# Kernel tuning notes

Measured on AMD Instinct MI355X. Metric: run time of the kernel, lower is better.

The kernel has to match this reference:

```python
import jax, jax.numpy as jnp
import numpy as np

B, L, D, H = 4, 2048, 2048, 16
HEAD_DIM = D // H
EPS = 1e-5


def rmsnorm(x, w):
    # fp32 RMSNorm as in the torch module
    xf = x.astype(jnp.float32)
    rms = jnp.sqrt(jnp.mean(xf * xf, axis=-1, keepdims=True) + EPS)
    return xf / rms * w


def apply_rope(x, freqs):
    # x: (..., D) with interleaved even/odd pairs; freqs: (2, L, D/2) = (sin, cos)
    sin, cos = freqs[0], freqs[1]
    xr = x.reshape(*x.shape[:-1], D // 2, 2)
    x_even, x_odd = xr[..., 0], xr[..., 1]
    e = x_even * cos - x_odd * sin
    o = x_odd * cos + x_even * sin
    return jnp.stack([e, o], axis=-1).reshape(x.shape)


def setup_inputs() -> dict:
    key = jax.random.key(0)
    k0, k1, k2 = jax.random.split(key, 3)
    x_BLD = jax.random.normal(k0, (B, L, D), dtype=jnp.float32)
    # realistic RoPE angle table over the full dim (matches module usage)
    t = jnp.arange(L, dtype=jnp.float32)[:, None]
    inv_freq = 1.0 / (10000.0 ** (jnp.arange(D // 2, dtype=jnp.float32) / (D // 2)))
    ang = t * inv_freq[None, :]                      # (L, D/2)
    freqs = jnp.stack([jnp.sin(ang), jnp.cos(ang)])  # (2, L, D/2)
    wqkv = jax.random.normal(k1, (3 * D, D), dtype=jnp.float32) * 0.02
    wo = jax.random.normal(k2, (D, D), dtype=jnp.float32) * 0.02
    q_norm_w = jnp.ones((D,), dtype=jnp.float32)
    k_norm_w = jnp.ones((D,), dtype=jnp.float32)
    return {"x_BLD": x_BLD, "freqs": freqs, "wqkv": wqkv, "wo": wo,
            "q_norm_w": q_norm_w, "k_norm_w": k_norm_w}


def reference(x_BLD, freqs, wqkv, wo, q_norm_w, k_norm_w):
    dtype = x_BLD.dtype
    qkv = x_BLD @ wqkv.T                             # (B, L, 3D)
    q, k, v = jnp.split(qkv, 3, axis=-1)
    q = apply_rope(rmsnorm(q, q_norm_w), freqs).astype(dtype)
    k = apply_rope(rmsnorm(k, k_norm_w), freqs).astype(dtype)
    # (B, L, D) -> (B, H, L, hd)
    q = q.reshape(B, L, H, HEAD_DIM).transpose(0, 2, 1, 3)
    k = k.reshape(B, L, H, HEAD_DIM).transpose(0, 2, 1, 3)
    v = v.reshape(B, L, H, HEAD_DIM).transpose(0, 2, 1, 3)
    scale = HEAD_DIM ** -0.5
    scores = jnp.einsum('bhqd,bhkd->bhqk', q, k) * scale
    attn = jax.nn.softmax(scores, axis=-1)
    out = jnp.einsum('bhqk,bhkd->bhqd', attn, v)
    out = out.transpose(0, 2, 1, 3).reshape(B, L, D)
    return out @ wo.T
```

## Files before the change

kernel.cpp:

```cpp
#include <hip/hip_runtime.h>
#include <stdint.h>
#include <stddef.h>

typedef unsigned short u16;
typedef __bf16 bf16x8 __attribute__((ext_vector_type(8)));
typedef float  f32x4  __attribute__((ext_vector_type(4)));
typedef float  f32x16 __attribute__((ext_vector_type(16)));

__device__ __forceinline__ float bf2f(u16 u){ return __uint_as_float(((unsigned)u)<<16); }
__device__ __forceinline__ u16 f2bf(float f){
  unsigned u = __float_as_uint(f);
  return (u16)((u + 0x7fffu + ((u>>16)&1u)) >> 16);
}
__device__ __forceinline__ void gl_lds16(const void* g, void* s){
  __builtin_amdgcn_global_load_lds(
      (__attribute__((address_space(1))) void*)(void*)g,
      (__attribute__((address_space(3))) void*)s, 16, 0, 0);
}

__global__ void k_f2bf(const float* __restrict__ in, u16* __restrict__ out, int n4){
  int i = blockIdx.x*256 + threadIdx.x;
  if (i < n4){
    float4 v = ((const float4*)in)[i];
    ((ushort4*)out)[i] = make_ushort4(f2bf(v.x), f2bf(v.y), f2bf(v.z), f2bf(v.w));
  }
}

template<int BF16OUT>
__global__ __launch_bounds__(256,2) void k_gemm_bt(const u16* __restrict__ A,
                                                   const u16* __restrict__ Bm,
                                                   void* __restrict__ Cout,
                                                   int M, int N, int K){
  __shared__ __align__(16) u16 As[128*64];
  __shared__ __align__(16) u16 Bs[128*64];
  const int tid = threadIdx.x, w = tid>>6, ln = tid&63;
  const int l16 = ln&15, quad = ln>>4;
  const int wm = w&1, wn = w>>1;
  const int m0 = blockIdx.y*128, n0 = blockIdx.x*128;
  const f32x4 z4 = {0.f,0.f,0.f,0.f};
  f32x4 acc[4][4];
  #pragma unroll
  for (int i=0;i<4;++i)
    #pragma unroll
    for (int j=0;j<4;++j) acc[i][j] = z4;

  const int nkb = K >> 6;
  for (int kb=0; kb<nkb; ++kb){
    __syncthreads();
    const int ka = kb*64;
    #pragma unroll
    for (int j=0;j<4;++j){
      gl_lds16(A  + (size_t)(m0 + w*32 + j*8 + (ln>>3))*K + ka + (ln&7)*8,
               &As[(w*32+j*8)*64]);
      gl_lds16(Bm + (size_t)(n0 + w*32 + j*8 + (ln>>3))*K + ka + (ln&7)*8,
               &Bs[(w*32+j*8)*64]);
    }
    __builtin_amdgcn_s_waitcnt(0);
    __syncthreads();
    #pragma unroll
    for (int k0=0;k0<64;k0+=32){
      bf16x8 a[4], b[4];
      #pragma unroll
      for (int mt=0;mt<4;++mt) a[mt] = *(const bf16x8*)&As[(wm*64+mt*16+l16)*64 + k0 + quad*8];
      #pragma unroll
      for (int nt=0;nt<4;++nt) b[nt] = *(const bf16x8*)&Bs[(wn*64+nt*16+l16)*64 + k0 + quad*8];
      #pragma unroll
      for (int mt=0;mt<4;++mt)
        #pragma unroll
        for (int nt=0;nt<4;++nt)
          acc[mt][nt] = __builtin_amdgcn_mfma_f32_16x16x32_bf16(a[mt], b[nt], acc[mt][nt], 0,0,0);
    }
  }
  #pragma unroll
  for (int mt=0;mt<4;++mt)
    #pragma unroll
    for (int nt=0;nt<4;++nt)
      #pragma unroll
      for (int j=0;j<4;++j){
        int row = m0 + wm*64 + mt*16 + quad*4 + j;
        int col = n0 + wn*64 + nt*16 + l16;
        if (BF16OUT) ((u16*)Cout)[(size_t)row*N + col] = f2bf(acc[mt][nt][j]);
        else         ((float*)Cout)[(size_t)row*N + col] = acc[mt][nt][j];
      }
}

__global__ void k_prep_qk(const u16* __restrict__ qkv, const float* __restrict__ freqs,
                          const float* __restrict__ qw, const float* __restrict__ kw,
                          u16* __restrict__ Qo, u16* __restrict__ Ko){
  const int row = blockIdx.x;
  const int b = row >> 11, l = row & 2047;
  const int tid = threadIdx.x;
  const u16* qr = qkv + (size_t)row*6144;
  float qe[4], qo[4], ke[4], ko_[4];
  float sq = 0.f, sk = 0.f;
  #pragma unroll
  for (int it=0; it<4; ++it){
    int p = tid + it*256;
    ushort2 q2 = ((const ushort2*)qr)[p];
    ushort2 k2 = ((const ushort2*)(qr+2048))[p];
    qe[it]=bf2f(q2.x); qo[it]=bf2f(q2.y);
    ke[it]=bf2f(k2.x); ko_[it]=bf2f(k2.y);
    sq += qe[it]*qe[it] + qo[it]*qo[it];
    sk += ke[it]*ke[it] + ko_[it]*ko_[it];
  }
  #pragma unroll
  for (int off=32; off; off>>=1){ sq += __shfl_xor(sq, off); sk += __shfl_xor(sk, off); }
  __shared__ float red[8];
  if ((tid&63)==0){ red[tid>>6]=sq; red[4+(tid>>6)]=sk; }
  __syncthreads();
  sq = red[0]+red[1]+red[2]+red[3];
  sk = red[4]+red[5]+red[6]+red[7];
  const float rq = rsqrtf(sq*(1.f/2048.f) + 1e-5f);
  const float rk = rsqrtf(sk*(1.f/2048.f) + 1e-5f);
  const float QS = 0.08838834764831845f * 1.4426950408889634f;
  #pragma unroll
  for (int it=0; it<4; ++it){
    int p = tid + it*256;
    float sn = freqs[(size_t)l*1024 + p];
    float cs = freqs[2097152 + (size_t)l*1024 + p];
    float2 w2q = ((const float2*)qw)[p];
    float2 w2k = ((const float2*)kw)[p];
    int h = p>>6, dd2 = p&63;
    size_t o = ((size_t)(b*16+h)*2048 + l)*64 + dd2;
    float a = qe[it]*rq*w2q.x, c = qo[it]*rq*w2q.y;
    ((ushort2*)Qo)[o] = make_ushort2(f2bf((a*cs - c*sn)*QS), f2bf((c*cs + a*sn)*QS));
    a = ke[it]*rk*w2k.x; c = ko_[it]*rk*w2k.y;
    ((ushort2*)Ko)[o] = make_ushort2(f2bf(a*cs - c*sn), f2bf(c*cs + a*sn));
  }
}

__global__ void k_prep_v(const u16* __restrict__ qkv, u16* __restrict__ Vt){
  const int lt = blockIdx.x, bh = blockIdx.y;
  const int b = bh>>4, h = bh&15;
  __shared__ u16 tile[64][136];
  const int tid = threadIdx.x;
  #pragma unroll
  for (int it=0; it<32; ++it){
    int idx = it*256 + tid;
    int lo = idx >> 7, dd = idx & 127;
    tile[lo][dd] = qkv[(size_t)(b*2048 + lt*64 + lo)*6144 + 4096 + h*128 + dd];
  }
  __syncthreads();
  #pragma unroll
  for (int it=0; it<32; ++it){
    int idx = it*256 + tid;
    int dd = idx >> 6, lo = idx & 63;
    Vt[((size_t)bh*128 + dd)*2048 + lt*64 + lo] = tile[lo][dd];
  }
}

__global__ __launch_bounds__(256,2) void k_flash(const u16* __restrict__ Q,
                                                 const u16* __restrict__ Kg,
                                                 const u16* __restrict__ Vt,
                                                 u16* __restrict__ O){
  __shared__ __align__(16) u16 Kt[128*136];
  __shared__ __align__(16) u16 Vs[128*136];
  const int qt = blockIdx.x, bh = blockIdx.y;
  const int tid = threadIdx.x, w = tid>>6, ln = tid&63;
  const int l31 = ln&31, hi = ln>>5;
  const int b = bh>>4, h = bh&15;
  const size_t qkbase = (size_t)bh*(2048*128);

  const int srow = tid>>4, scol = tid&15;
  const u16* kgp = Kg + qkbase + (size_t)srow*128 + scol*8;
  const u16* vgp = Vt + (size_t)bh*(128*2048) + (size_t)srow*2048 + scol*8;
  u16* kld = &Kt[srow*136 + scol*8];
  u16* vld = &Vs[srow*136 + scol*8];

  bf16x8 qf[8];
  {
    const u16* qp = Q + qkbase + (size_t)(qt*128 + w*32 + l31)*128 + hi*8;
    #pragma unroll
    for (int kk=0; kk<8; ++kk) qf[kk] = *(const bf16x8*)(qp + kk*16);
  }

  f32x16 o[4];
  #pragma unroll
  for (int dt=0; dt<4; ++dt)
    #pragma unroll
    for (int r=0; r<16; ++r) o[dt][r] = 0.f;
  float l_ = 0.f;

  bf16x8 kreg[8], vreg[8];
  #pragma unroll
  for (int it=0; it<8; ++it) kreg[it] = *(const bf16x8*)(kgp + (size_t)it*16*128);
  #pragma unroll
  for (int it=0; it<8; ++it) vreg[it] = *(const bf16x8*)(vgp + (size_t)it*16*2048);

  union U4 { unsigned u[4]; bf16x8 v; };

  for (int kt=0; kt<16; ++kt){
    __syncthreads();
    #pragma unroll
    for (int it=0; it<8; ++it) *(bf16x8*)(kld + it*16*136) = kreg[it];
    #pragma unroll
    for (int it=0; it<8; ++it) *(bf16x8*)(vld + it*16*136) = vreg[it];
    __syncthreads();
    if (kt < 15){
      #pragma unroll
      for (int it=0; it<8; ++it)
        kreg[it] = *(const bf16x8*)(kgp + (size_t)(kt+1)*128*128 + (size_t)it*16*128);
      #pragma unroll
      for (int it=0; it<8; ++it)
        vreg[it] = *(const bf16x8*)(vgp + (kt+1)*128 + (size_t)it*16*2048);
    }
    f32x16 s[4];
    #pragma unroll
    for (int t=0;t<4;++t)
      #pragma unroll
      for (int r=0;r<16;++r) s[t][r] = 0.f;
    #pragma unroll
    for (int kk=0; kk<8; ++kk){
      #pragma unroll
      for (int t=0; t<4; ++t){
        bf16x8 a = *(const bf16x8*)&Kt[(t*32 + l31)*136 + kk*16 + hi*8];
        s[t] = __builtin_amdgcn_mfma_f32_32x32x16_bf16(a, qf[kk], s[t], 0,0,0);
      }
    }
    float rs = 0.f;
    bf16x8 bfrag[8];
    #pragma unroll
    for (int t=0;t<4;++t){
      unsigned pk[4][2];
      #pragma unroll
      for (int g=0;g<4;++g){
        float p0 = exp2f(s[t][g*4+0] - 8.0f);
        float p1 = exp2f(s[t][g*4+1] - 8.0f);
        float p2 = exp2f(s[t][g*4+2] - 8.0f);
        float p3 = exp2f(s[t][g*4+3] - 8.0f);
        rs += (p0+p1)+(p2+p3);
        pk[g][0] = (unsigned)f2bf(p0) | ((unsigned)f2bf(p1)<<16);
        pk[g][1] = (unsigned)f2bf(p2) | ((unsigned)f2bf(p3)<<16);
      }
      unsigned a0 = (unsigned)__shfl_xor((int)(hi ? pk[0][0] : pk[1][0]), 32);
      unsigned a1 = (unsigned)__shfl_xor((int)(hi ? pk[0][1] : pk[1][1]), 32);
      unsigned b0 = (unsigned)__shfl_xor((int)(hi ? pk[2][0] : pk[3][0]), 32);
      unsigned b1 = (unsigned)__shfl_xor((int)(hi ? pk[2][1] : pk[3][1]), 32);
      U4 u0, u1;
      u0.u[0] = hi ? a0       : pk[0][0];
      u0.u[1] = hi ? a1       : pk[0][1];
      u0.u[2] = hi ? pk[1][0] : a0;
      u0.u[3] = hi ? pk[1][1] : a1;
      u1.u[0] = hi ? b0       : pk[2][0];
      u1.u[1] = hi ? b1       : pk[2][1];
      u1.u[2] = hi ? pk[3][0] : b0;
      u1.u[3] = hi ? pk[3][1] : b1;
      bfrag[t*2+0] = u0.v;
      bfrag[t*2+1] = u1.v;
    }
    rs += __shfl_xor(rs, 32);
    l_ += rs;
    #pragma unroll
    for (int kk=0; kk<8; ++kk){
      #pragma unroll
      for (int dt=0; dt<4; ++dt){
        bf16x8 a = *(const bf16x8*)&Vs[(dt*32 + l31)*136 + kk*16 + hi*8];
        o[dt] = __builtin_amdgcn_mfma_f32_32x32x16_bf16(a, bfrag[kk], o[dt], 0,0,0);
      }
    }
  }
  const float inv = 1.f/l_;
  __syncthreads();
  #pragma unroll
  for (int dt=0;dt<4;++dt)
    #pragma unroll
    for (int g=0;g<4;++g)
      *(ushort4*)&Kt[(w*32+l31)*136 + dt*32 + g*8 + hi*4] =
        make_ushort4(f2bf(o[dt][g*4+0]*inv), f2bf(o[dt][g*4+1]*inv),
                     f2bf(o[dt][g*4+2]*inv), f2bf(o[dt][g*4+3]*inv));
  __syncthreads();
  #pragma unroll
  for (int it=0; it<8; ++it){
    int q = it*16 + srow;
    bf16x8 vv = *(const bf16x8*)&Kt[q*136 + scol*8];
    *(bf16x8*)&O[(size_t)(b*2048 + qt*128 + q)*2048 + h*128 + scol*8] = vv;
  }
}

extern "C" void kernel_launch(void* const* d_in, const int* in_sizes, int n_in,
                              void* d_out, int out_size, void* d_ws, size_t ws_size,
                              hipStream_t stream){
  const float* x     = (const float*)d_in[0];
  const float* freqs = (const float*)d_in[1];
  const float* wqkv  = (const float*)d_in[2];
  const float* wo    = (const float*)d_in[3];
  const float* qw    = (const float*)d_in[4];
  const float* kw    = (const float*)d_in[5];
  char* ws = (char*)d_ws;
  u16* xbf    = (u16*)(ws);
  u16* wqkvbf = (u16*)(ws + 33554432);
  u16* wobf   = (u16*)(ws + 58720256);
  u16* qkvbf  = (u16*)(ws + 67108864);
  u16* Qbf    = (u16*)(ws + 167772160);
  u16* Kbf    = (u16*)(ws + 201326592);
  u16* Vtbf   = (u16*)(ws + 234881024);
  u16* Abf    = qkvbf;
  float* out  = (float*)d_out;

  k_f2bf<<<16384,256,0,stream>>>(x,    xbf,    4194304);
  k_f2bf<<<12288,256,0,stream>>>(wqkv, wqkvbf, 3145728);
  k_f2bf<<< 4096,256,0,stream>>>(wo,   wobf,   1048576);
  k_gemm_bt<1><<<dim3(48,64),256,0,stream>>>(xbf, wqkvbf, qkvbf, 8192, 6144, 2048);
  k_prep_qk<<<8192,256,0,stream>>>(qkvbf, freqs, qw, kw, Qbf, Kbf);
  k_prep_v<<<dim3(32,64),256,0,stream>>>(qkvbf, Vtbf);
  k_flash<<<dim3(16,64),256,0,stream>>>(Qbf, Kbf, Vtbf, Abf);
  k_gemm_bt<0><<<dim3(16,64),256,0,stream>>>(Abf, wobf, out, 8192, 2048, 2048);
}
```

Measured before the change: 740.9 us.

## Replace GEMM with 256x256-tile, 8-wave, double-buffered pipelined kernel

Replaces the 128x128 single-buffered bf16 GEMM with a 256x256 tile kernel using 512 threads. Global-to-LDS loads of the next K slices are interleaved with MFMA work on quarter-tiles, using partial vmcnt waits and barriers. The LDS layout is XOR-swizzled to avoid bank conflicts, workgroup order is remapped for L2 locality, and MFMA issue priority is raised with s_setprio. The cost targeted is the load/compute serialisation and low reuse of the old loop. In exchange it uses 128KB of LDS per block and a more fragile barrier schedule.

Result: faster. 698.2 us (-5.8%).

```diff
diff --git a/kernel.cpp b/kernel.cpp
--- a/kernel.cpp
+++ b/kernel.cpp
@@ -26,62 +26,115 @@
   }
 }
 
+#define BAR()  do{ __asm__ __volatile__("" ::: "memory"); \
+                   __builtin_amdgcn_s_barrier(); \
+                   __asm__ __volatile__("" ::: "memory"); }while(0)
+#define LGKM0() __asm__ __volatile__("s_waitcnt lgkmcnt(0)" ::: "memory")
+#define VMC4()  __asm__ __volatile__("s_waitcnt vmcnt(4)" ::: "memory")
+#define VMC0()  __asm__ __volatile__("s_waitcnt vmcnt(0)" ::: "memory")
+
+#define STAGE_A(B_,H_,T_) do{ \
+  const u16* _s = A + (size_t)(m0 + (H_)*128 + w16 + sr)*K + (T_)*64 + sc; \
+  gl_lds16(_s,               &As[B_][H_][w16*64]); \
+  gl_lds16(_s + (size_t)8*K, &As[B_][H_][(w16+8)*64]); }while(0)
+#define STAGE_B(B_,H_,T_) do{ \
+  const u16* _s = Bm + (size_t)(n0 + (H_)*128 + w16 + sr)*K + (T_)*64 + sc; \
+  gl_lds16(_s,               &Bs[B_][H_][w16*64]); \
+  gl_lds16(_s + (size_t)8*K, &Bs[B_][H_][(w16+8)*64]); }while(0)
+
+#define RD_A(H_,B_) do{ \
+  _Pragma("unroll") for (int mt=0; mt<4; ++mt){ \
+    int r_ = wm*64 + mt*16 + l16; const u16* p_ = &As[B_][H_][r_*64]; \
+    af[mt][0] = *(const bf16x8*)&p_[(( quad    ^ (r_&7))<<3)]; \
+    af[mt][1] = *(const bf16x8*)&p_[(((quad+4) ^ (r_&7))<<3)]; } }while(0)
+#define RD_B(H_,B_) do{ \
+  _Pragma("unroll") for (int nt=0; nt<2; ++nt){ \
+    int r_ = wn*32 + nt*16 + l16; const u16* p_ = &Bs[B_][H_][r_*64]; \
+    bfr[nt][0] = *(const bf16x8*)&p_[(( quad    ^ (r_&7))<<3)]; \
+    bfr[nt][1] = *(const bf16x8*)&p_[(((quad+4) ^ (r_&7))<<3)]; } }while(0)
+
+#define MM(QM,QN) do{ \
+  LGKM0(); \
+  __builtin_amdgcn_s_setprio(1); \
+  _Pragma("unroll") for (int k_=0;k_<2;++k_) \
+    _Pragma("unroll") for (int mt=0;mt<4;++mt) \
+      _Pragma("unroll") for (int nt=0;nt<2;++nt) \
+        acc[QM][QN][mt][nt] = __builtin_amdgcn_mfma_f32_16x16x32_bf16( \
+            af[mt][k_], bfr[nt][k_], acc[QM][QN][mt][nt], 0,0,0); \
+  __builtin_amdgcn_s_setprio(0); }while(0)
+
 template<int BF16OUT>
-__global__ __launch_bounds__(256,2) void k_gemm_bt(const u16* __restrict__ A,
+__global__ __launch_bounds__(512,2) void k_gemm256(const u16* __restrict__ A,
                                                    const u16* __restrict__ Bm,
                                                    void* __restrict__ Cout,
                                                    int M, int N, int K){
-  __shared__ __align__(16) u16 As[128*64];
-  __shared__ __align__(16) u16 Bs[128*64];
+  __shared__ __align__(16) u16 As[2][2][128*64];
+  __shared__ __align__(16) u16 Bs[2][2][128*64];
   const int tid = threadIdx.x, w = tid>>6, ln = tid&63;
   const int l16 = ln&15, quad = ln>>4;
   const int wm = w&1, wn = w>>1;
-  const int m0 = blockIdx.y*128, n0 = blockIdx.x*128;
-  const f32x4 z4 = {0.f,0.f,0.f,0.f};
-  f32x4 acc[4][4];
-  #pragma unroll
-  for (int i=0;i<4;++i)
-    #pragma unroll
-    for (int j=0;j<4;++j) acc[i][j] = z4;
-
-  const int nkb = K >> 6;
-  for (int kb=0; kb<nkb; ++kb){
-    __syncthreads();
-    const int ka = kb*64;
-    #pragma unroll
-    for (int j=0;j<4;++j){
-      gl_lds16(A  + (size_t)(m0 + w*32 + j*8 + (ln>>3))*K + ka + (ln&7)*8,
-               &As[(w*32+j*8)*64]);
-      gl_lds16(Bm + (size_t)(n0 + w*32 + j*8 + (ln>>3))*K + ka + (ln&7)*8,
-               &Bs[(w*32+j*8)*64]);
-    }
-    __builtin_amdgcn_s_waitcnt(0);
-    __syncthreads();
-    #pragma unroll
-    for (int k0=0;k0<64;k0+=32){
-      bf16x8 a[4], b[4];
-      #pragma unroll
-      for (int mt=0;mt<4;++mt) a[mt] = *(const bf16x8*)&As[(wm*64+mt*16+l16)*64 + k0 + quad*8];
-      #pragma unroll
-      for (int nt=0;nt<4;++nt) b[nt] = *(const bf16x8*)&Bs[(wn*64+nt*16+l16)*64 + k0 + quad*8];
+  const int w16 = w*16, sr = ln>>3;
+  const int sc = ((ln&7) ^ sr) << 3;
+  const int nbx = N>>8;
+  const int nwg = nbx*(M>>8);
+  const int lid = blockIdx.y*nbx + blockIdx.x;
+  const int swz = (lid&7)*(nwg>>3) + (lid>>3);
+  const int m0 = (swz/nbx)<<8, n0 = (swz%nbx)<<8;
+
+  f32x4 acc[2][2][4][2];
+  #pragma unroll
+  for (int a=0;a<2;++a)
+    #pragma unroll
+    for (int b=0;b<2;++b)
+      #pragma unroll
+      for (int c=0;c<4;++c)
+        #pragma unroll
+        for (int d=0;d<2;++d){ acc[a][b][c][d][0]=0.f; acc[a][b][c][d][1]=0.f;
+                               acc[a][b][c][d][2]=0.f; acc[a][b][c][d][3]=0.f; }
+  bf16x8 af[4][2], bfr[2][2];
+
+  STAGE_A(0,0,0); STAGE_B(0,0,0); STAGE_A(0,1,0); STAGE_B(0,1,0);
+  STAGE_B(1,0,1); STAGE_A(1,1,1);
+  VMC4(); BAR();
+
+  const int niter = K>>7;
+  for (int j=0; j<niter-1; ++j){
+    const int t1 = 2*j+1;
+    RD_A(0,0); RD_B(0,0); STAGE_A(1,0,t1);           BAR(); MM(0,0); BAR();
+    RD_A(1,0);            STAGE_B(1,1,t1);           BAR(); MM(1,0); BAR();
+    RD_B(1,0);            STAGE_B(0,0,t1+1);         BAR(); MM(1,1); BAR();
+    RD_A(0,0);            STAGE_A(0,1,t1+1); VMC4(); BAR(); MM(0,1); BAR();
+    RD_A(0,1); RD_B(0,1); STAGE_A(0,0,t1+1);         BAR(); MM(0,0); BAR();
+    RD_A(1,1);            STAGE_B(0,1,t1+1);         BAR(); MM(1,0); BAR();
+    RD_B(1,1);            STAGE_B(1,0,t1+2);         BAR(); MM(1,1); BAR();
+    RD_A(0,1);            STAGE_A(1,1,t1+2); VMC4(); BAR(); MM(0,1); BAR();
+  }
+  {
+    const int T1 = 2*niter-1;
+    RD_A(0,0); RD_B(0,0); STAGE_A(1,0,T1);           BAR(); MM(0,0); BAR();
+    RD_A(1,0);            STAGE_B(1,1,T1);           BAR(); MM(1,0); BAR();
+    RD_B(1,0);                                       BAR(); MM(1,1); BAR();
+    RD_A(0,0);                               VMC0(); BAR(); MM(0,1); BAR();
+    RD_A(0,1); RD_B(0,1);                            BAR(); MM(0,0); BAR();
+    RD_A(1,1);                                       BAR(); MM(1,0); BAR();
+    RD_B(1,1);                                       BAR(); MM(1,1); BAR();
+    RD_A(0,1);                                       BAR(); MM(0,1); BAR();
+  }
+  #pragma unroll
+  for (int qm=0;qm<2;++qm)
+    #pragma unroll
+    for (int qn=0;qn<2;++qn)
       #pragma unroll
       for (int mt=0;mt<4;++mt)
         #pragma unroll
-        for (int nt=0;nt<4;++nt)
-          acc[mt][nt] = __builtin_amdgcn_mfma_f32_16x16x32_bf16(a[mt], b[nt], acc[mt][nt], 0,0,0);
-    }
-  }
-  #pragma unroll
-  for (int mt=0;mt<4;++mt)
-    #pragma unroll
-    for (int nt=0;nt<4;++nt)
-      #pragma unroll
-      for (int j=0;j<4;++j){
-        int row = m0 + wm*64 + mt*16 + quad*4 + j;
-        int col = n0 + wn*64 + nt*16 + l16;
-        if (BF16OUT) ((u16*)Cout)[(size_t)row*N + col] = f2bf(acc[mt][nt][j]);
-        else         ((float*)Cout)[(size_t)row*N + col] = acc[mt][nt][j];
-      }
+        for (int nt=0;nt<2;++nt)
+          #pragma unroll
+          for (int jj=0;jj<4;++jj){
+            int row = m0 + qm*128 + wm*64 + mt*16 + quad*4 + jj;
+            int col = n0 + qn*128 + wn*32 + nt*16 + l16;
+            if (BF16OUT) ((u16*)Cout)[(size_t)row*N + col] = f2bf(acc[qm][qn][mt][nt][jj]);
+            else         ((float*)Cout)[(size_t)row*N + col] = acc[qm][qn][mt][nt][jj];
+          }
 }
 
 __global__ void k_prep_qk(const u16* __restrict__ qkv, const float* __restrict__ freqs,
@@ -300,9 +353,9 @@
   k_f2bf<<<16384,256,0,stream>>>(x,    xbf,    4194304);
   k_f2bf<<<12288,256,0,stream>>>(wqkv, wqkvbf, 3145728);
   k_f2bf<<< 4096,256,0,stream>>>(wo,   wobf,   1048576);
-  k_gemm_bt<1><<<dim3(48,64),256,0,stream>>>(xbf, wqkvbf, qkvbf, 8192, 6144, 2048);
+  k_gemm256<1><<<dim3(24,32),512,0,stream>>>(xbf, wqkvbf, qkvbf, 8192, 6144, 2048);
   k_prep_qk<<<8192,256,0,stream>>>(qkvbf, freqs, qw, kw, Qbf, Kbf);
   k_prep_v<<<dim3(32,64),256,0,stream>>>(qkvbf, Vtbf);
   k_flash<<<dim3(16,64),256,0,stream>>>(Qbf, Kbf, Vtbf, Abf);
-  k_gemm_bt<0><<<dim3(16,64),256,0,stream>>>(Abf, wobf, out, 8192, 2048, 2048);
-}
+  k_gemm256<0><<<dim3(8,32),512,0,stream>>>(Abf, wobf, out, 8192, 2048, 2048);
+}
```
